# Kernel optimization log

Hardware: AMD Instinct MI355X
Metric: run time of the kernel (lower is better)

## Reference

```python
import jax, jax.numpy as jnp
import numpy as np

N = 50000      # nodes
E = 800000     # edges (avg degree 16)
IN, EMB, HID, OUT = 128, 256, 256, 128
KS = (25000, 12500)  # absolute top-k node counts per pooling level
NEG = -1e9


def setup_inputs() -> dict:
    key = jax.random.key(0)
    k = jax.random.split(key, 20)
    s = 0.05
    rn = lambda kk, shp: (jax.random.normal(kk, shp, jnp.float32) * s)
    return {
        "features": jax.random.normal(k[0], (N, IN), jnp.float32),
        "src": jax.random.randint(k[1], (E,), 0, N, dtype=jnp.int32),
        "dst": jax.random.randint(k[2], (E,), 0, N, dtype=jnp.int32),
        "W_embed": rn(k[3], (IN, EMB)), "b_embed": jnp.zeros((EMB,), jnp.float32),
        "W_enc0": rn(k[4], (EMB, HID)), "b_enc0": jnp.zeros((HID,), jnp.float32),
        "W_enc1": rn(k[5], (HID, HID)), "b_enc1": jnp.zeros((HID,), jnp.float32),
        "W_p0": rn(k[6], (HID, 1)), "b_p0": jnp.zeros((1,), jnp.float32),
        "W_p1": rn(k[7], (HID, 1)), "b_p1": jnp.zeros((1,), jnp.float32),
        "W_bot": rn(k[8], (HID, HID)), "b_bot": jnp.zeros((HID,), jnp.float32),
        "W_dec0": rn(k[9], (HID, HID)), "b_dec0": jnp.zeros((HID,), jnp.float32),
        "W_dec1": rn(k[10], (HID, OUT)), "b_dec1": jnp.zeros((OUT,), jnp.float32),
    }


def _gcn(h, src, dst, emask, W, b, act):
    """DGL GraphConv, norm='both': D_out^{-1/2} A D_in^{-1/2} h W + b, deg clamped >=1.
    emask: float [E] validity mask for edges of the current (sub)graph."""
    n = h.shape[0]
    deg_out = jnp.clip(jax.ops.segment_sum(emask, src, num_segments=n), 1.0)
    deg_in = jnp.clip(jax.ops.segment_sum(emask, dst, num_segments=n), 1.0)
    msg = (h * (deg_out ** -0.5)[:, None])[src] * emask[:, None]  # [E, F]
    agg = jax.ops.segment_sum(msg, dst, num_segments=n)
    out = (agg * (deg_in ** -0.5)[:, None]) @ W + b
    return jax.nn.relu(out) if act else out


def _forward(features, src, dst, W_embed, b_embed, W_enc0, b_enc0, W_enc1, b_enc1,
             W_p0, b_p0, W_p1, b_p1, W_bot, b_bot, W_dec0, b_dec0, W_dec1, b_dec1):
    n = features.shape[0]
    ones_e = jnp.ones((src.shape[0],), features.dtype)
    enc = [(W_enc0, b_enc0), (W_enc1, b_enc1)]
    pools = [(W_p0, b_p0), (W_p1, b_p1)]
    dec = [(W_dec0, b_dec0), (W_dec1, b_dec1)]
    L = len(KS)

    h = _gcn(features, src, dst, ones_e, W_embed, b_embed, True)
    masks = [jnp.ones((n,), features.dtype)]  # node mask per graph level
    hidden = []
    for i in range(L):  # encoder (dropout = eval-mode identity)
        m = masks[i]
        em = m[src] * m[dst]
        h = _gcn(h, src, dst, em, enc[i][0], enc[i][1], True) * m[:, None]
        hidden.append(h)
        # gPool: sigmoid projection score, top-k node selection, gate by score
        scores = jax.nn.sigmoid(h @ pools[i][0] + pools[i][1])[:, 0]
        _, idx = jax.lax.top_k(jnp.where(m > 0, scores, NEG), KS[i])
        nm = jnp.zeros((n,), features.dtype).at[idx].set(1.0)
        h = h * (scores * nm)[:, None]
        masks.append(nm)
    mL = masks[L]
    emL = mL[src] * mL[dst]
    h = _gcn(h, src, dst, emL, W_bot, b_bot, True) * mL[:, None]
    for i in range(L):  # decoder: gUnpool (identity under full-rep masking) + skip + GCN
        j = L - 1 - i
        h = h + hidden[j]
        m = masks[j]
        em = m[src] * m[dst]
        act = i < L - 1  # last decoder layer has no activation
        h = _gcn(h, src, dst, em, dec[i][0], dec[i][1], act) * m[:, None]
    return h


def reference(features, src, dst, W_embed, b_embed, W_enc0, b_enc0, W_enc1, b_enc1,
              W_p0, b_p0, W_p1, b_p1, W_bot, b_bot, W_dec0, b_dec0, W_dec1, b_dec1):
    return _forward(features, src, dst, W_embed, b_embed, W_enc0, b_enc0, W_enc1, b_enc1,
                    W_p0, b_p0, W_p1, b_p1, W_bot, b_bot, W_dec0, b_dec0, W_dec1, b_dec1)
```

## Files before the change

kernel.cpp:

```cpp
#include <hip/hip_runtime.h>
#include <hip/hip_bf16.h>
#include <type_traits>

__global__ void hist_kernel(const int* __restrict__ src, const int* __restrict__ dst,
                            int* __restrict__ deg_out, int* __restrict__ deg_in, int E) {
    int e = blockIdx.x * blockDim.x + threadIdx.x;
    if (e < E) {
        atomicAdd(&deg_out[src[e]], 1);
        atomicAdd(&deg_in[dst[e]], 1);
    }
}

__global__ void scan_kernel(const int* __restrict__ deg, int* __restrict__ row_ptr,
                            int* __restrict__ cursor, int n) {
    __shared__ int wsum[16];
    __shared__ int running;
    int tid = threadIdx.x, lane = tid & 63, wid = tid >> 6;
    if (tid == 0) running = 0;
    __syncthreads();
    for (int base = 0; base < n; base += 1024) {
        int i = base + tid;
        int v = (i < n) ? deg[i] : 0;
        int incl = v;
        #pragma unroll
        for (int off = 1; off < 64; off <<= 1) {
            int t = __shfl_up(incl, off);
            if (lane >= off) incl += t;
        }
        if (lane == 63) wsum[wid] = incl;
        __syncthreads();
        if (wid == 0 && lane < 16) {
            int s = wsum[lane], si = s;
            #pragma unroll
            for (int off = 1; off < 16; off <<= 1) {
                int t = __shfl_up(si, off);
                if (lane >= off) si += t;
            }
            wsum[lane] = si - s;
        }
        __syncthreads();
        int excl = running + wsum[wid] + (incl - v);
        if (i < n) { row_ptr[i] = excl; cursor[i] = excl; }
        __syncthreads();
        if (tid == 1023) running = excl + v;
        __syncthreads();
    }
    if (tid == 0) row_ptr[n] = running;
}

__global__ void fill_kernel(const int* __restrict__ src, const int* __restrict__ dst,
                            int* __restrict__ cursor, int* __restrict__ col, int E) {
    int e = blockIdx.x * blockDim.x + threadIdx.x;
    if (e < E) {
        int p = atomicAdd(&cursor[dst[e]], 1);
        col[p] = src[e];
    }
}

__global__ void sort_rows_kernel(const int* __restrict__ row_ptr, int* __restrict__ col, int n) {
    int v = blockIdx.x * blockDim.x + threadIdx.x;
    if (v >= n) return;
    int e0 = row_ptr[v], e1 = row_ptr[v + 1];
    for (int i = e0 + 1; i < e1; ++i) {
        int key = col[i];
        int j = i - 1;
        while (j >= e0 && col[j] > key) { col[j + 1] = col[j]; --j; }
        col[j + 1] = key;
    }
}

__global__ void out_deg_mask_kernel(const int* __restrict__ src, const int* __restrict__ dst,
                                    const float* __restrict__ m, float* __restrict__ so, int E) {
    int e = blockIdx.x * blockDim.x + threadIdx.x;
    if (e < E) {
        float md = m[dst[e]];
        if (md != 0.f) atomicAdd(&so[src[e]], md);
    }
}

__global__ void in_deg_mask_kernel(const int* __restrict__ row_ptr, const int* __restrict__ col,
                                   const float* __restrict__ m, float* __restrict__ si, int n) {
    int v = blockIdx.x * blockDim.x + threadIdx.x;
    if (v < n) {
        float s = 0.f;
        int e1 = row_ptr[v + 1];
        for (int e = row_ptr[v]; e < e1; ++e) s += m[col[e]];
        si[v] = s;
    }
}

__global__ void scale_full_kernel(const int* __restrict__ dout, const int* __restrict__ din,
                                  float* __restrict__ s, float* __restrict__ t, int n) {
    int v = blockIdx.x * blockDim.x + threadIdx.x;
    if (v < n) {
        s[v] = 1.f / sqrtf((float)max(dout[v], 1));
        t[v] = 1.f / sqrtf((float)max(din[v], 1));
    }
}

__global__ void scale_mask_kernel(const float* __restrict__ gate, const float* __restrict__ mask,
                                  const float* __restrict__ so, const float* __restrict__ si,
                                  float* __restrict__ s, float* __restrict__ t, int n) {
    int v = blockIdx.x * blockDim.x + threadIdx.x;
    if (v < n) {
        s[v] = gate[v] * (1.f / sqrtf(fmaxf(so[v], 1.f)));
        t[v] = mask[v] * (1.f / sqrtf(fmaxf(si[v], 1.f)));
    }
}

__global__ void agg_feat_128_kernel(const int* __restrict__ row_ptr, const int* __restrict__ col,
                                    const float* __restrict__ X, const float* __restrict__ s,
                                    const float* __restrict__ t, float* __restrict__ out, int n) {
    int tid = threadIdx.x;
    int node = blockIdx.x * 8 + (tid >> 5);
    int f4 = tid & 31;
    if (node >= n) return;
    int e0 = row_ptr[node], e1 = row_ptr[node + 1];
    const float4* X4 = (const float4*)X;
    float ax = 0.f, ay = 0.f, az = 0.f, aw = 0.f;
    int e = e0;
    for (; e + 3 < e1; e += 4) {
        int u0 = col[e], u1 = col[e + 1], u2 = col[e + 2], u3 = col[e + 3];
        float s0 = s[u0], s1 = s[u1], s2 = s[u2], s3 = s[u3];
        float4 x0 = X4[(size_t)u0 * 32 + f4];
        float4 x1 = X4[(size_t)u1 * 32 + f4];
        float4 x2 = X4[(size_t)u2 * 32 + f4];
        float4 x3 = X4[(size_t)u3 * 32 + f4];
        ax += s0 * x0.x; ay += s0 * x0.y; az += s0 * x0.z; aw += s0 * x0.w;
        ax += s1 * x1.x; ay += s1 * x1.y; az += s1 * x1.z; aw += s1 * x1.w;
        ax += s2 * x2.x; ay += s2 * x2.y; az += s2 * x2.z; aw += s2 * x2.w;
        ax += s3 * x3.x; ay += s3 * x3.y; az += s3 * x3.z; aw += s3 * x3.w;
    }
    for (; e < e1; ++e) {
        int u = col[e];
        float sc = s[u];
        float4 q = X4[(size_t)u * 32 + f4];
        ax += sc * q.x; ay += sc * q.y; az += sc * q.z; aw += sc * q.w;
    }
    float tv = t[node];
    float4 r; r.x = ax * tv; r.y = ay * tv; r.z = az * tv; r.w = aw * tv;
    ((float4*)out)[(size_t)node * 32 + f4] = r;
}

template <bool MASKED>
__global__ void agg_f32_256_kernel(const int* __restrict__ row_ptr, const int* __restrict__ col,
                                   const float* __restrict__ X, const float* __restrict__ s,
                                   const float* __restrict__ t, float* __restrict__ out, int n) {
    int tid = threadIdx.x;
    int node = blockIdx.x * 4 + (tid >> 6);
    int f4 = tid & 63;
    if (node >= n) return;
    float tv = t[node];
    if (MASKED && tv == 0.f) return;
    int e0 = row_ptr[node], e1 = row_ptr[node + 1];
    const float4* X4 = (const float4*)X;
    float ax = 0.f, ay = 0.f, az = 0.f, aw = 0.f;
    int e = e0;
    for (; e + 3 < e1; e += 4) {
        int u0 = col[e], u1 = col[e + 1], u2 = col[e + 2], u3 = col[e + 3];
        float s0 = s[u0], s1 = s[u1], s2 = s[u2], s3 = s[u3];
        if (!MASKED) {
            float4 x0 = X4[(size_t)u0 * 64 + f4];
            float4 x1 = X4[(size_t)u1 * 64 + f4];
            float4 x2 = X4[(size_t)u2 * 64 + f4];
            float4 x3 = X4[(size_t)u3 * 64 + f4];
            ax += s0 * x0.x; ay += s0 * x0.y; az += s0 * x0.z; aw += s0 * x0.w;
            ax += s1 * x1.x; ay += s1 * x1.y; az += s1 * x1.z; aw += s1 * x1.w;
            ax += s2 * x2.x; ay += s2 * x2.y; az += s2 * x2.z; aw += s2 * x2.w;
            ax += s3 * x3.x; ay += s3 * x3.y; az += s3 * x3.z; aw += s3 * x3.w;
        } else {
            if (s0 != 0.f) { float4 x = X4[(size_t)u0 * 64 + f4];
                ax += s0 * x.x; ay += s0 * x.y; az += s0 * x.z; aw += s0 * x.w; }
            if (s1 != 0.f) { float4 x = X4[(size_t)u1 * 64 + f4];
                ax += s1 * x.x; ay += s1 * x.y; az += s1 * x.z; aw += s1 * x.w; }
            if (s2 != 0.f) { float4 x = X4[(size_t)u2 * 64 + f4];
                ax += s2 * x.x; ay += s2 * x.y; az += s2 * x.z; aw += s2 * x.w; }
            if (s3 != 0.f) { float4 x = X4[(size_t)u3 * 64 + f4];
                ax += s3 * x.x; ay += s3 * x.y; az += s3 * x.z; aw += s3 * x.w; }
        }
    }
    for (; e < e1; ++e) {
        int u = col[e];
        float sc = s[u];
        if (!MASKED || sc != 0.f) {
            float4 xv = X4[(size_t)u * 64 + f4];
            ax += sc * xv.x; ay += sc * xv.y; az += sc * xv.z; aw += sc * xv.w;
        }
    }
    float4 r; r.x = ax * tv; r.y = ay * tv; r.z = az * tv; r.w = aw * tv;
    ((float4*)out)[(size_t)node * 64 + f4] = r;
}

__global__ void agg_bias_128_kernel(const int* __restrict__ row_ptr, const int* __restrict__ col,
                                    const float* __restrict__ P, const float* __restrict__ t,
                                    const float* __restrict__ bias, float* __restrict__ out, int n) {
    int tid = threadIdx.x;
    int node = blockIdx.x * 8 + (tid >> 5);
    int f4 = tid & 31;
    if (node >= n) return;
    int e0 = row_ptr[node], e1 = row_ptr[node + 1];
    const float4* P4 = (const float4*)P;
    float ax = 0.f, ay = 0.f, az = 0.f, aw = 0.f;
    int e = e0;
    for (; e + 3 < e1; e += 4) {
        int u0 = col[e], u1 = col[e + 1], u2 = col[e + 2], u3 = col[e + 3];
        float4 x0 = P4[(size_t)u0 * 32 + f4];
        float4 x1 = P4[(size_t)u1 * 32 + f4];
        float4 x2 = P4[(size_t)u2 * 32 + f4];
        float4 x3 = P4[(size_t)u3 * 32 + f4];
        ax += x0.x; ay += x0.y; az += x0.z; aw += x0.w;
        ax += x1.x; ay += x1.y; az += x1.z; aw += x1.w;
        ax += x2.x; ay += x2.y; az += x2.z; aw += x2.w;
        ax += x3.x; ay += x3.y; az += x3.z; aw += x3.w;
    }
    for (; e < e1; ++e) {
        int u = col[e];
        float4 q = P4[(size_t)u * 32 + f4];
        ax += q.x; ay += q.y; az += q.z; aw += q.w;
    }
    float tv = t[node];
    float4 bv = ((const float4*)bias)[f4];
    float4 r;
    r.x = ax * tv + bv.x; r.y = ay * tv + bv.y;
    r.z = az * tv + bv.z; r.w = aw * tv + bv.w;
    ((float4*)out)[(size_t)node * 32 + f4] = r;
}

template <bool RELU>
__global__ __launch_bounds__(256) void gemm_kernel(const float* __restrict__ A,
                                                   const float* __restrict__ W,
                                                   const float* __restrict__ bias,
                                                   const float* __restrict__ mask,
                                                   const float* __restrict__ rowscale,
                                                   float* __restrict__ C, int M, int K, int Nn) {
    __shared__ float As[16][68];
    __shared__ float Bs[16][132];
    int tid = threadIdx.x;
    int bm = blockIdx.x * 64, bn = blockIdx.y * 128;
    int mA = tid >> 2, kqA = (tid & 3) * 4;
    int kB = tid >> 4, nqB = (tid & 15) * 8;
    int tm = (tid >> 4) * 4, tn = (tid & 15) * 4;
    float acc[4][8] = {};
    float rs = rowscale ? rowscale[bm + mA] : 1.f;
    for (int k0 = 0; k0 < K; k0 += 16) {
        float4 av = *(const float4*)(A + (size_t)(bm + mA) * K + k0 + kqA);
        As[kqA + 0][mA] = av.x * rs; As[kqA + 1][mA] = av.y * rs;
        As[kqA + 2][mA] = av.z * rs; As[kqA + 3][mA] = av.w * rs;
        const float* wp = W + (size_t)(k0 + kB) * Nn + bn + nqB;
        *(float4*)&Bs[kB][nqB]     = *(const float4*)wp;
        *(float4*)&Bs[kB][nqB + 4] = *(const float4*)(wp + 4);
        __syncthreads();
        #pragma unroll
        for (int kk = 0; kk < 16; ++kk) {
            float4 a  = *(const float4*)&As[kk][tm];
            float4 b0 = *(const float4*)&Bs[kk][tn];
            float4 b1 = *(const float4*)&Bs[kk][tn + 64];
            float ar[4] = {a.x, a.y, a.z, a.w};
            float br[8] = {b0.x, b0.y, b0.z, b0.w, b1.x, b1.y, b1.z, b1.w};
            #pragma unroll
            for (int i2 = 0; i2 < 4; i2++)
                #pragma unroll
                for (int j = 0; j < 8; j++) acc[i2][j] += ar[i2] * br[j];
        }
        __syncthreads();
    }
    #pragma unroll
    for (int i2 = 0; i2 < 4; i2++) {
        int row = bm + tm + i2;
        if (row < M) {
            float mv = mask ? mask[row] : 1.f;
            float o[8];
            #pragma unroll
            for (int j = 0; j < 8; j++) {
                int cj = (j < 4) ? (tn + j) : (64 + tn + j - 4);
                float x = acc[i2][j] + (bias ? bias[bn + cj] : 0.f);
                if (RELU) x = fmaxf(x, 0.f);
                o[j] = x * mv;
            }
            float* cp = C + (size_t)row * Nn + bn;
            *(float4*)(cp + tn)      = make_float4(o[0], o[1], o[2], o[3]);
            *(float4*)(cp + 64 + tn) = make_float4(o[4], o[5], o[6], o[7]);
        }
    }
}

template <bool RELU>
__global__ __launch_bounds__(256) void gemm_rows_kernel(const float* __restrict__ A,
                                                        const float* __restrict__ W,
                                                        const float* __restrict__ bias,
                                                        const int* __restrict__ idx, int Mc,
                                                        float* __restrict__ C, int K, int Nn) {
    __shared__ float As[16][68];
    __shared__ float Bs[16][132];
    __shared__ int ridx[64];
    int tid = threadIdx.x;
    int bm = blockIdx.x * 64, bn = blockIdx.y * 128;
    if (tid < 64) {
        int r = bm + tid;
        ridx[tid] = (r < Mc) ? idx[r] : idx[0];
    }
    __syncthreads();
    int mA = tid >> 2, kqA = (tid & 3) * 4;
    int kB = tid >> 4, nqB = (tid & 15) * 8;
    int tm = (tid >> 4) * 4, tn = (tid & 15) * 4;
    int rA = ridx[mA];
    float acc[4][8] = {};
    for (int k0 = 0; k0 < K; k0 += 16) {
        float4 av = *(const float4*)(A + (size_t)rA * K + k0 + kqA);
        As[kqA + 0][mA] = av.x; As[kqA + 1][mA] = av.y;
        As[kqA + 2][mA] = av.z; As[kqA + 3][mA] = av.w;
        const float* wp = W + (size_t)(k0 + kB) * Nn + bn + nqB;
        *(float4*)&Bs[kB][nqB]     = *(const float4*)wp;
        *(float4*)&Bs[kB][nqB + 4] = *(const float4*)(wp + 4);
        __syncthreads();
        #pragma unroll
        for (int kk = 0; kk < 16; ++kk) {
            float4 a  = *(const float4*)&As[kk][tm];
            float4 b0 = *(const float4*)&Bs[kk][tn];
            float4 b1 = *(const float4*)&Bs[kk][tn + 64];
            float ar[4] = {a.x, a.y, a.z, a.w};
            float br[8] = {b0.x, b0.y, b0.z, b0.w, b1.x, b1.y, b1.z, b1.w};
            #pragma unroll
            for (int i2 = 0; i2 < 4; i2++)
                #pragma unroll
                for (int j = 0; j < 8; j++) acc[i2][j] += ar[i2] * br[j];
        }
        __syncthreads();
    }
    #pragma unroll
    for (int i2 = 0; i2 < 4; i2++) {
        int r = bm + tm + i2;
        if (r < Mc) {
            int row = ridx[tm + i2];
            float o[8];
            #pragma unroll
            for (int j = 0; j < 8; j++) {
                int cj = (j < 4) ? (tn + j) : (64 + tn + j - 4);
                float x = acc[i2][j] + bias[bn + cj];
                if (RELU) x = fmaxf(x, 0.f);
                o[j] = x;
            }
            float* cp = C + (size_t)row * Nn + bn;
            *(float4*)(cp + tn)      = make_float4(o[0], o[1], o[2], o[3]);
            *(float4*)(cp + 64 + tn) = make_float4(o[4], o[5], o[6], o[7]);
        }
    }
}

__global__ void score_kernel(const float* __restrict__ H, const float* __restrict__ Wp,
                             const float* __restrict__ bp, const float* __restrict__ mask,
                             float* __restrict__ scores, float* __restrict__ keys, int n) {
    int lane = threadIdx.x & 63;
    int node = blockIdx.x * 4 + (threadIdx.x >> 6);
    if (node >= n) return;
    float4 hv = ((const float4*)(H + (size_t)node * 256))[lane];
    float4 wq = ((const float4*)Wp)[lane];
    float d = hv.x * wq.x + hv.y * wq.y + hv.z * wq.z + hv.w * wq.w;
    #pragma unroll
    for (int off = 32; off > 0; off >>= 1) d += __shfl_down(d, off);
    if (lane == 0) {
        float sc = 1.f / (1.f + expf(-(d + bp[0])));
        scores[node] = sc;
        keys[node] = (mask && mask[node] == 0.f) ? -1e9f : sc;
    }
}

__device__ __forceinline__ unsigned key_u(float f) {
    unsigned u = __float_as_uint(f);
    return (u & 0x80000000u) ? ~u : (u | 0x80000000u);
}

__device__ __forceinline__ void wave_hist_add(int* __restrict__ hist, unsigned bin, bool valid) {
    int lane = threadIdx.x & 63;
    while (true) {
        unsigned long long vmask = __ballot(valid);
        if (vmask == 0ull) break;
        int leader = __ffsll((long long)vmask) - 1;
        unsigned lbin = (unsigned)__shfl((int)bin, leader);
        bool match = valid && (bin == lbin);
        unsigned long long mmask = __ballot(match);
        if (lane == leader) atomicAdd(&hist[lbin], __popcll(mmask));
        if (match) valid = false;
    }
}

__global__ void topk_kernel(const float* __restrict__ keys, const float* __restrict__ scores,
                            float* __restrict__ nm, float* __restrict__ gate, int n, int K) {
    __shared__ int hist[256];
    __shared__ unsigned sh_prefix;
    __shared__ int sh_krem;
    __shared__ int sh_running;
    __shared__ int wsum[16];
    int tid = threadIdx.x, lane = tid & 63, wid = tid >> 6;
    if (tid == 0) { sh_prefix = 0u; sh_krem = K; sh_running = 0; }
    __syncthreads();
    for (int pass = 0; pass < 4; ++pass) {
        int shift = 24 - pass * 8;
        if (tid < 256) hist[tid] = 0;
        __syncthreads();
        unsigned pmask = (pass == 0) ? 0u : (0xFFFFFFFFu << (shift + 8));
        unsigned prefix = sh_prefix;
        for (int i = tid; i < n; i += 1024) {
            unsigned u = key_u(keys[i]);
            if ((u & pmask) == prefix) atomicAdd(&hist[(u >> shift) & 0xFF], 1);
        }
        __syncthreads();
        if (tid == 0) {
            int krem = sh_krem;
            int b;
            for (b = 255; b > 0; --b) {
                int c = hist[b];
                if (c >= krem) break;
                krem -= c;
            }
            sh_prefix = prefix | ((unsigned)b << shift);
            sh_krem = krem;
        }
        __syncthreads();
    }
    unsigned Tkey = sh_prefix;
    int need_eq = sh_krem;
    for (int base = 0; base < n; base += 1024) {
        int i = base + tid;
        unsigned u = 0; int flagv = 0;
        if (i < n) { u = key_u(keys[i]); flagv = (u == Tkey) ? 1 : 0; }
        unsigned long long bal = __ballot(flagv);
        int rank_w = __popcll(bal & ((1ull << lane) - 1ull));
        if (lane == 63) wsum[wid] = __popcll(bal);
        __syncthreads();
        int woff = 0;
        for (int w = 0; w < wid; ++w) woff += wsum[w];
        int grank = sh_running + woff + rank_w;
        if (i < n) {
            float v = (u > Tkey) ? 1.f : ((flagv && grank < need_eq) ? 1.f : 0.f);
            nm[i] = v;
            gate[i] = v * scores[i];
        }
        __syncthreads();
        if (tid == 0) {
            int tot = 0;
            for (int w = 0; w < 16; ++w) tot += wsum[w];
            sh_running += tot;
        }
        __syncthreads();
    }
}

__global__ void topk_hist1(const float* __restrict__ keys, int n, int* __restrict__ hist) {
    int i = blockIdx.x * blockDim.x + threadIdx.x;
    unsigned bin = 0; bool valid = (i < n);
    if (valid) bin = key_u(keys[i]) >> 16;
    wave_hist_add(hist, bin, valid);
}

__global__ void topk_scan1(const int* __restrict__ hist, int K, int* __restrict__ sel) {
    __shared__ int arr[1024];
    int tid = threadIdx.x;
    int base = tid * 64;
    int local = 0;
    #pragma unroll 8
    for (int b = 0; b < 64; ++b) local += hist[base + b];
    arr[tid] = local;
    __syncthreads();
    for (int off = 1; off < 1024; off <<= 1) {
        int v = (tid + off < 1024) ? arr[tid + off] : 0;
        __syncthreads();
        arr[tid] += v;
        __syncthreads();
    }
    int above = arr[tid] - local;
    if (above < K && arr[tid] >= K) {
        int run = above;
        for (int b = base + 63; b >= base; --b) {
            int c = hist[b];
            if (run + c >= K) { sel[0] = b; sel[1] = K - run; break; }
            run += c;
        }
    }
}

__global__ void topk_hist2(const float* __restrict__ keys, int n, const int* __restrict__ sel,
                           int* __restrict__ hist) {
    int i = blockIdx.x * blockDim.x + threadIdx.x;
    unsigned bin = 0; bool valid = false;
    if (i < n) {
        unsigned u = key_u(keys[i]);
        if ((int)(u >> 16) == sel[0]) { bin = u & 0xFFFF; valid = true; }
    }
    wave_hist_add(hist, bin, valid);
}

__global__ void topk_scan2(const int* __restrict__ hist, int* __restrict__ sel,
                           int* __restrict__ tie_cnt) {
    __shared__ int arr[1024];
    int tid = threadIdx.x;
    if (tid == 0) *tie_cnt = 0;
    int K = sel[1];
    int base = tid * 64;
    int local = 0;
    #pragma unroll 8
    for (int b = 0; b < 64; ++b) local += hist[base + b];
    arr[tid] = local;
    __syncthreads();
    for (int off = 1; off < 1024; off <<= 1) {
        int v = (tid + off < 1024) ? arr[tid + off] : 0;
        __syncthreads();
        arr[tid] += v;
        __syncthreads();
    }
    int above = arr[tid] - local;
    if (above < K && arr[tid] >= K) {
        int run = above;
        for (int b = base + 63; b >= base; --b) {
            int c = hist[b];
            if (run + c >= K) {
                sel[2] = (int)((((unsigned)sel[0]) << 16) | (unsigned)b);
                sel[3] = K - run;
                break;
            }
            run += c;
        }
    }
}

__global__ void topk_mark(const float* __restrict__ keys, const float* __restrict__ scores,
                          const int* __restrict__ sel, float* __restrict__ nm,
                          float* __restrict__ gate, int* __restrict__ tie_list,
                          int* __restrict__ tie_cnt, int n) {
    int i = blockIdx.x * blockDim.x + threadIdx.x;
    if (i >= n) return;
    unsigned Tkey = (unsigned)sel[2];
    unsigned u = key_u(keys[i]);
    float v = 0.f;
    if (u > Tkey) v = 1.f;
    else if (u == Tkey) { int p = atomicAdd(tie_cnt, 1); tie_list[p] = i; }
    nm[i] = v;
    gate[i] = v * scores[i];
}

__global__ void topk_ties(const float* __restrict__ scores, const int* __restrict__ sel,
                          const int* __restrict__ tie_list, const int* __restrict__ tie_cnt,
                          float* __restrict__ nm, float* __restrict__ gate) {
    int cnt = *tie_cnt;
    int need = sel[3];
    for (int j = threadIdx.x; j < cnt; j += blockDim.x) {
        int idx = tie_list[j];
        int rank = 0;
        for (int k2 = 0; k2 < cnt; ++k2) rank += (tie_list[k2] < idx) ? 1 : 0;
        if (rank < need) { nm[idx] = 1.f; gate[idx] = scores[idx]; }
    }
}

__global__ void compact_kernel(const float* __restrict__ nm, int* __restrict__ idx,
                               int* __restrict__ cnt, int n) {
    int i = blockIdx.x * blockDim.x + threadIdx.x;
    if (i < n && nm[i] != 0.f) {
        int p = atomicAdd(cnt, 1);
        idx[p] = i;
    }
}

__global__ void add_mask_kernel(float* __restrict__ A, const float* __restrict__ B,
                                const float* __restrict__ mask, int n4) {
    int i = blockIdx.x * blockDim.x + threadIdx.x;
    if (i < n4) {
        float4 a = ((float4*)A)[i];
        float4 b = ((const float4*)B)[i];
        if (mask && mask[i >> 6] == 0.f) { a.x = 0.f; a.y = 0.f; a.z = 0.f; a.w = 0.f; }
        a.x += b.x; a.y += b.y; a.z += b.z; a.w += b.w;
        ((float4*)A)[i] = a;
    }
}

extern "C" void kernel_launch(void* const* d_in, const int* in_sizes, int n_in,
                              void* d_out, int out_size, void* d_ws, size_t ws_size,
                              hipStream_t stream) {
    const int n = in_sizes[0] / 128;
    const int E = in_sizes[1];
    const int NPAD = ((n + 63) / 64) * 64;
    const int K1 = 25000, K2 = 12500;

    const float* features = (const float*)d_in[0];
    const int* src = (const int*)d_in[1];
    const int* dst = (const int*)d_in[2];
    const float* W_embed = (const float*)d_in[3];
    const float* b_embed = (const float*)d_in[4];
    const float* W_enc0  = (const float*)d_in[5];
    const float* b_enc0  = (const float*)d_in[6];
    const float* W_enc1  = (const float*)d_in[7];
    const float* b_enc1  = (const float*)d_in[8];
    const float* W_p0    = (const float*)d_in[9];
    const float* b_p0    = (const float*)d_in[10];
    const float* W_p1    = (const float*)d_in[11];
    const float* b_p1    = (const float*)d_in[12];
    const float* W_bot   = (const float*)d_in[13];
    const float* b_bot   = (const float*)d_in[14];
    const float* W_dec0  = (const float*)d_in[15];
    const float* b_dec0  = (const float*)d_in[16];
    const float* W_dec1  = (const float*)d_in[17];
    const float* b_dec1  = (const float*)d_in[18];
    float* out_f = (float*)d_out;

    char* ws = (char*)d_ws;
    size_t off = 0;
    auto alloc = [&](size_t bytes) -> void* {
        void* p = ws + off;
        off += (bytes + 255) & ~(size_t)255;
        return p;
    };
    (void)alloc(256);
    int* row_ptr  = (int*)alloc((size_t)(n + 1) * 4);
    int* cursor   = (int*)alloc((size_t)n * 4);
    int* col      = (int*)alloc((size_t)E * 4);
    int* deg_out_i= (int*)alloc((size_t)n * 4);
    int* deg_in_i = (int*)alloc((size_t)n * 4);
    float* so_m1  = (float*)alloc((size_t)n * 4);
    float* si_m1  = (float*)alloc((size_t)n * 4);
    float* so_m2  = (float*)alloc((size_t)n * 4);
    float* si_m2  = (float*)alloc((size_t)n * 4);
    float* sarr   = (float*)alloc((size_t)n * 4);
    float* tarr   = (float*)alloc((size_t)n * 4);
    float* scores1= (float*)alloc((size_t)n * 4);
    float* keys1  = (float*)alloc((size_t)n * 4);
    float* scores2= (float*)alloc((size_t)n * 4);
    float* keys2  = (float*)alloc((size_t)n * 4);
    float* nm1    = (float*)alloc((size_t)n * 4);
    float* gate1  = (float*)alloc((size_t)n * 4);
    float* nm2    = (float*)alloc((size_t)n * 4);
    float* gate2  = (float*)alloc((size_t)n * 4);
    size_t big = (size_t)NPAD * 256 * 4;
    float* A = (float*)alloc(big);
    float* B = (float*)alloc(big);
    float* C = (float*)alloc(big);
    float* D = (float*)alloc(big);
    int* rhist    = (int*)alloc(65536 * 4);
    int* sel      = (int*)alloc(256);
    int* tie_cnt  = (int*)alloc(256);
    int* tie_list = (int*)alloc((size_t)n * 4);
    float* s0     = (float*)alloc((size_t)n * 4);
    float* t0     = (float*)alloc((size_t)n * 4);
    int* idx1     = (int*)alloc((size_t)n * 4);
    int* idx2     = (int*)alloc((size_t)n * 4);
    int* ccnt     = (int*)alloc(256);
    bool fast = (off <= ws_size);

    dim3 blk(256);
    int gE = (E + 255) / 256;
    int gN = (n + 255) / 256;
    int gAgg256 = (n + 3) / 4;
    int gAgg128 = (n + 7) / 8;
    int gScore = (n + 3) / 4;
    dim3 gemm_g(NPAD / 64, 2);
    dim3 gemm_g128(NPAD / 64, 1);
    dim3 gemm_gK1((K1 + 63) / 64, 2);
    dim3 gemm_gK2((K2 + 63) / 64, 2);
    int gAdd = (n * 64 + 255) / 256;

    auto run_topk = [&](const float* keys, const float* scores, float* nm, float* gate, int K) {
        if (fast) {
            hipMemsetAsync(rhist, 0, 65536 * 4, stream);
            topk_hist1<<<gN, blk, 0, stream>>>(keys, n, rhist);
            topk_scan1<<<1, 1024, 0, stream>>>(rhist, K, sel);
            hipMemsetAsync(rhist, 0, 65536 * 4, stream);
            topk_hist2<<<gN, blk, 0, stream>>>(keys, n, sel, rhist);
            topk_scan2<<<1, 1024, 0, stream>>>(rhist, sel, tie_cnt);
            topk_mark<<<gN, blk, 0, stream>>>(keys, scores, sel, nm, gate, tie_list, tie_cnt, n);
            topk_ties<<<1, 256, 0, stream>>>(scores, sel, tie_list, tie_cnt, nm, gate);
        } else {
            topk_kernel<<<1, 1024, 0, stream>>>(keys, scores, nm, gate, n, K);
        }
    };
    float* sF = fast ? s0 : sarr;
    float* tF = fast ? t0 : tarr;

    hipMemsetAsync(deg_out_i, 0, (size_t)n * 4, stream);
    hipMemsetAsync(deg_in_i, 0, (size_t)n * 4, stream);
    hist_kernel<<<gE, blk, 0, stream>>>(src, dst, deg_out_i, deg_in_i, E);
    scan_kernel<<<1, 1024, 0, stream>>>(deg_in_i, row_ptr, cursor, n);
    fill_kernel<<<gE, blk, 0, stream>>>(src, dst, cursor, col, E);
    sort_rows_kernel<<<gN, blk, 0, stream>>>(row_ptr, col, n);

    scale_full_kernel<<<gN, blk, 0, stream>>>(deg_out_i, deg_in_i, sF, tF, n);

    agg_feat_128_kernel<<<gAgg128, blk, 0, stream>>>(row_ptr, col, features, sF, tF, D, n);
    gemm_kernel<true><<<gemm_g, blk, 0, stream>>>(D, W_embed, b_embed, nullptr, nullptr, A, n, 128, 256);

    agg_f32_256_kernel<false><<<gAgg256, blk, 0, stream>>>(row_ptr, col, A, sF, tF, D, n);
    gemm_kernel<true><<<gemm_g, blk, 0, stream>>>(D, W_enc0, b_enc0, nullptr, nullptr, B, n, 256, 256);

    score_kernel<<<gScore, blk, 0, stream>>>(B, W_p0, b_p0, nullptr, scores1, keys1, n);
    run_topk(keys1, scores1, nm1, gate1, K1);
    if (fast) {
        hipMemsetAsync(ccnt, 0, 4, stream);
        compact_kernel<<<gN, blk, 0, stream>>>(nm1, idx1, ccnt, n);
    }

    hipMemsetAsync(so_m1, 0, (size_t)n * 4, stream);
    out_deg_mask_kernel<<<gE, blk, 0, stream>>>(src, dst, nm1, so_m1, E);
    in_deg_mask_kernel<<<gN, blk, 0, stream>>>(row_ptr, col, nm1, si_m1, n);
    scale_mask_kernel<<<gN, blk, 0, stream>>>(gate1, nm1, so_m1, si_m1, sarr, tarr, n);
    agg_f32_256_kernel<true><<<gAgg256, blk, 0, stream>>>(row_ptr, col, B, sarr, tarr, D, n);
    if (fast)
        gemm_rows_kernel<true><<<gemm_gK1, blk, 0, stream>>>(D, W_enc1, b_enc1, idx1, K1, C, 256, 256);
    else
        gemm_kernel<true><<<gemm_g, blk, 0, stream>>>(D, W_enc1, b_enc1, nm1, nullptr, C, n, 256, 256);

    score_kernel<<<gScore, blk, 0, stream>>>(C, W_p1, b_p1, nm1, scores2, keys2, n);
    run_topk(keys2, scores2, nm2, gate2, K2);
    if (fast) {
        hipMemsetAsync(ccnt + 1, 0, 4, stream);
        compact_kernel<<<gN, blk, 0, stream>>>(nm2, idx2, ccnt + 1, n);
    }

    hipMemsetAsync(so_m2, 0, (size_t)n * 4, stream);
    out_deg_mask_kernel<<<gE, blk, 0, stream>>>(src, dst, nm2, so_m2, E);
    in_deg_mask_kernel<<<gN, blk, 0, stream>>>(row_ptr, col, nm2, si_m2, n);
    scale_mask_kernel<<<gN, blk, 0, stream>>>(gate2, nm2, so_m2, si_m2, sarr, tarr, n);
    agg_f32_256_kernel<true><<<gAgg256, blk, 0, stream>>>(row_ptr, col, C, sarr, tarr, D, n);
    if (fast)
        gemm_rows_kernel<true><<<gemm_gK2, blk, 0, stream>>>(D, W_bot, b_bot, idx2, K2, A, 256, 256);
    else
        gemm_kernel<true><<<gemm_g, blk, 0, stream>>>(D, W_bot, b_bot, nm2, nullptr, A, n, 256, 256);

    add_mask_kernel<<<gAdd, blk, 0, stream>>>(A, C, fast ? nm2 : nullptr, n * 64);
    scale_mask_kernel<<<gN, blk, 0, stream>>>(nm1, nm1, so_m1, si_m1, sarr, tarr, n);
    agg_f32_256_kernel<true><<<gAgg256, blk, 0, stream>>>(row_ptr, col, A, sarr, tarr, D, n);
    if (fast)
        gemm_rows_kernel<true><<<gemm_gK1, blk, 0, stream>>>(D, W_dec0, b_dec0, idx1, K1, A, 256, 256);
    else
        gemm_kernel<true><<<gemm_g, blk, 0, stream>>>(D, W_dec0, b_dec0, nm1, nullptr, A, n, 256, 256);

    add_mask_kernel<<<gAdd, blk, 0, stream>>>(A, B, fast ? nm1 : nullptr, n * 64);
    if (!fast)
        scale_full_kernel<<<gN, blk, 0, stream>>>(deg_out_i, deg_in_i, sarr, tarr, n);
    gemm_kernel<false><<<gemm_g128, blk, 0, stream>>>(A, W_dec1, nullptr, nullptr, sF, C, n, 256, 128);
    agg_bias_128_kernel<<<gAgg128, blk, 0, stream>>>(row_ptr, col, C, tF, b_dec1, out_f, n);

    (void)n_in; (void)out_size;
}
```

Measured before the change: 1.312 ms.

## Aggregate only selected rows, build CSR by source, fuse compaction into top-k

Adds a source-sorted CSR so masked out-degrees can be computed by gather inside one fused deg_scale kernel, replacing the atomic edge pass, a memset and separate in-degree and scale kernels. Aggregation now runs only over the compacted top-k node indices instead of all n nodes. Compaction is folded into topk_mark and topk_ties, and the histogram is cleared inside the scan kernels instead of by memsets. The cost is an extra scan and fill to build the second CSR, plus nondeterministic order of the compacted index list.

```diff
diff --git a/kernel.cpp b/kernel.cpp
--- a/kernel.cpp
+++ b/kernel.cpp
@@ -48,12 +48,12 @@
     if (tid == 0) row_ptr[n] = running;
 }
 
-__global__ void fill_kernel(const int* __restrict__ src, const int* __restrict__ dst,
+__global__ void fill_kernel(const int* __restrict__ a, const int* __restrict__ b,
                             int* __restrict__ cursor, int* __restrict__ col, int E) {
     int e = blockIdx.x * blockDim.x + threadIdx.x;
     if (e < E) {
-        int p = atomicAdd(&cursor[dst[e]], 1);
-        col[p] = src[e];
+        int p = atomicAdd(&cursor[b[e]], 1);
+        col[p] = a[e];
     }
 }
 
@@ -106,6 +106,25 @@
         s[v] = gate[v] * (1.f / sqrtf(fmaxf(so[v], 1.f)));
         t[v] = mask[v] * (1.f / sqrtf(fmaxf(si[v], 1.f)));
     }
+}
+
+__global__ void deg_scale_kernel(const int* __restrict__ rp_s, const int* __restrict__ cs,
+                                 const int* __restrict__ rp_d, const int* __restrict__ cd,
+                                 const float* __restrict__ gate, const float* __restrict__ mask,
+                                 float* __restrict__ s, float* __restrict__ t,
+                                 float* __restrict__ so_out, float* __restrict__ si_out, int n) {
+    int v = blockIdx.x * blockDim.x + threadIdx.x;
+    if (v >= n) return;
+    float so = 0.f;
+    int e1 = rp_s[v + 1];
+    for (int e = rp_s[v]; e < e1; ++e) so += mask[cs[e]];
+    float si = 0.f;
+    e1 = rp_d[v + 1];
+    for (int e = rp_d[v]; e < e1; ++e) si += mask[cd[e]];
+    s[v] = gate[v] * (1.f / sqrtf(fmaxf(so, 1.f)));
+    t[v] = mask[v] * (1.f / sqrtf(fmaxf(si, 1.f)));
+    so_out[v] = so;
+    si_out[v] = si;
 }
 
 __global__ void agg_feat_128_kernel(const int* __restrict__ row_ptr, const int* __restrict__ col,
@@ -191,6 +210,44 @@
     ((float4*)out)[(size_t)node * 64 + f4] = r;
 }
 
+__global__ void agg_rows_256_kernel(const int* __restrict__ row_ptr, const int* __restrict__ col,
+                                    const float* __restrict__ X, const float* __restrict__ s,
+                                    const float* __restrict__ t, const int* __restrict__ idx,
+                                    int Mc, float* __restrict__ out) {
+    int tid = threadIdx.x;
+    int li = blockIdx.x * 4 + (tid >> 6);
+    int f4 = tid & 63;
+    if (li >= Mc) return;
+    int node = idx[li];
+    float tv = t[node];
+    int e0 = row_ptr[node], e1 = row_ptr[node + 1];
+    const float4* X4 = (const float4*)X;
+    float ax = 0.f, ay = 0.f, az = 0.f, aw = 0.f;
+    int e = e0;
+    for (; e + 3 < e1; e += 4) {
+        int u0 = col[e], u1 = col[e + 1], u2 = col[e + 2], u3 = col[e + 3];
+        float s0 = s[u0], s1 = s[u1], s2 = s[u2], s3 = s[u3];
+        if (s0 != 0.f) { float4 x = X4[(size_t)u0 * 64 + f4];
+            ax += s0 * x.x; ay += s0 * x.y; az += s0 * x.z; aw += s0 * x.w; }
+        if (s1 != 0.f) { float4 x = X4[(size_t)u1 * 64 + f4];
+            ax += s1 * x.x; ay += s1 * x.y; az += s1 * x.z; aw += s1 * x.w; }
+        if (s2 != 0.f) { float4 x = X4[(size_t)u2 * 64 + f4];
+            ax += s2 * x.x; ay += s2 * x.y; az += s2 * x.z; aw += s2 * x.w; }
+        if (s3 != 0.f) { float4 x = X4[(size_t)u3 * 64 + f4];
+            ax += s3 * x.x; ay += s3 * x.y; az += s3 * x.z; aw += s3 * x.w; }
+    }
+    for (; e < e1; ++e) {
+        int u = col[e];
+        float sc = s[u];
+        if (sc != 0.f) {
+            float4 xv = X4[(size_t)u * 64 + f4];
+            ax += sc * xv.x; ay += sc * xv.y; az += sc * xv.z; aw += sc * xv.w;
+        }
+    }
+    float4 r; r.x = ax * tv; r.y = ay * tv; r.z = az * tv; r.w = aw * tv;
+    ((float4*)out)[(size_t)node * 64 + f4] = r;
+}
+
 __global__ void agg_bias_128_kernel(const int* __restrict__ row_ptr, const int* __restrict__ col,
                                     const float* __restrict__ P, const float* __restrict__ t,
                                     const float* __restrict__ bias, float* __restrict__ out, int n) {
@@ -453,7 +510,7 @@
     wave_hist_add(hist, bin, valid);
 }
 
-__global__ void topk_scan1(const int* __restrict__ hist, int K, int* __restrict__ sel) {
+__global__ void topk_scan1(int* __restrict__ hist, int K, int* __restrict__ sel) {
     __shared__ int arr[1024];
     int tid = threadIdx.x;
     int base = tid * 64;
@@ -477,6 +534,8 @@
             run += c;
         }
     }
+    #pragma unroll 8
+    for (int b = 0; b < 64; ++b) hist[base + b] = 0;
 }
 
 __global__ void topk_hist2(const float* __restrict__ keys, int n, const int* __restrict__ sel,
@@ -490,11 +549,11 @@
     wave_hist_add(hist, bin, valid);
 }
 
-__global__ void topk_scan2(const int* __restrict__ hist, int* __restrict__ sel,
-                           int* __restrict__ tie_cnt) {
+__global__ void topk_scan2(int* __restrict__ hist, int* __restrict__ sel,
+                           int* __restrict__ tie_cnt, int* __restrict__ ccnt) {
     __shared__ int arr[1024];
     int tid = threadIdx.x;
-    if (tid == 0) *tie_cnt = 0;
+    if (tid == 0) { *tie_cnt = 0; *ccnt = 0; }
     int K = sel[1];
     int base = tid * 64;
     int local = 0;
@@ -521,18 +580,21 @@
             run += c;
         }
     }
+    #pragma unroll 8
+    for (int b = 0; b < 64; ++b) hist[base + b] = 0;
 }
 
 __global__ void topk_mark(const float* __restrict__ keys, const float* __restrict__ scores,
                           const int* __restrict__ sel, float* __restrict__ nm,
                           float* __restrict__ gate, int* __restrict__ tie_list,
-                          int* __restrict__ tie_cnt, int n) {
+                          int* __restrict__ tie_cnt, int* __restrict__ sidx,
+                          int* __restrict__ ccnt, int n) {
     int i = blockIdx.x * blockDim.x + threadIdx.x;
     if (i >= n) return;
     unsigned Tkey = (unsigned)sel[2];
     unsigned u = key_u(keys[i]);
     float v = 0.f;
-    if (u > Tkey) v = 1.f;
+    if (u > Tkey) { v = 1.f; int p = atomicAdd(ccnt, 1); sidx[p] = i; }
     else if (u == Tkey) { int p = atomicAdd(tie_cnt, 1); tie_list[p] = i; }
     nm[i] = v;
     gate[i] = v * scores[i];
@@ -540,23 +602,18 @@
 
 __global__ void topk_ties(const float* __restrict__ scores, const int* __restrict__ sel,
                           const int* __restrict__ tie_list, const int* __restrict__ tie_cnt,
-                          float* __restrict__ nm, float* __restrict__ gate) {
+                          float* __restrict__ nm, float* __restrict__ gate,
+                          int* __restrict__ sidx, int* __restrict__ ccnt) {
     int cnt = *tie_cnt;
     int need = sel[3];
     for (int j = threadIdx.x; j < cnt; j += blockDim.x) {
         int idx = tie_list[j];
         int rank = 0;
         for (int k2 = 0; k2 < cnt; ++k2) rank += (tie_list[k2] < idx) ? 1 : 0;
-        if (rank < need) { nm[idx] = 1.f; gate[idx] = scores[idx]; }
-    }
-}
-
-__global__ void compact_kernel(const float* __restrict__ nm, int* __restrict__ idx,
-                               int* __restrict__ cnt, int n) {
-    int i = blockIdx.x * blockDim.x + threadIdx.x;
-    if (i < n && nm[i] != 0.f) {
-        int p = atomicAdd(cnt, 1);
-        idx[p] = i;
+        if (rank < need) {
+            nm[idx] = 1.f; gate[idx] = scores[idx];
+            int p = atomicAdd(ccnt, 1); sidx[p] = idx;
+        }
     }
 }
 
@@ -642,6 +699,9 @@
     int* idx1     = (int*)alloc((size_t)n * 4);
     int* idx2     = (int*)alloc((size_t)n * 4);
     int* ccnt     = (int*)alloc(256);
+    int* row_ptr_s= (int*)alloc((size_t)(n + 1) * 4);
+    int* cursor_s = (int*)alloc((size_t)n * 4);
+    int* col_s    = (int*)alloc((size_t)E * 4);
     bool fast = (off <= ws_size);
 
     dim3 blk(256);
@@ -649,6 +709,8 @@
     int gN = (n + 255) / 256;
     int gAgg256 = (n + 3) / 4;
     int gAgg128 = (n + 7) / 8;
+    int gAggK1 = (K1 + 3) / 4;
+    int gAggK2 = (K2 + 3) / 4;
     int gScore = (n + 3) / 4;
     dim3 gemm_g(NPAD / 64, 2);
     dim3 gemm_g128(NPAD / 64, 1);
@@ -656,16 +718,16 @@
     dim3 gemm_gK2((K2 + 63) / 64, 2);
     int gAdd = (n * 64 + 255) / 256;
 
-    auto run_topk = [&](const float* keys, const float* scores, float* nm, float* gate, int K) {
+    auto run_topk = [&](const float* keys, const float* scores, float* nm, float* gate,
+                        int K, int* sidx, int* cc) {
         if (fast) {
-            hipMemsetAsync(rhist, 0, 65536 * 4, stream);
             topk_hist1<<<gN, blk, 0, stream>>>(keys, n, rhist);
             topk_scan1<<<1, 1024, 0, stream>>>(rhist, K, sel);
-            hipMemsetAsync(rhist, 0, 65536 * 4, stream);
             topk_hist2<<<gN, blk, 0, stream>>>(keys, n, sel, rhist);
-            topk_scan2<<<1, 1024, 0, stream>>>(rhist, sel, tie_cnt);
-            topk_mark<<<gN, blk, 0, stream>>>(keys, scores, sel, nm, gate, tie_list, tie_cnt, n);
-            topk_ties<<<1, 256, 0, stream>>>(scores, sel, tie_list, tie_cnt, nm, gate);
+            topk_scan2<<<1, 1024, 0, stream>>>(rhist, sel, tie_cnt, cc);
+            topk_mark<<<gN, blk, 0, stream>>>(keys, scores, sel, nm, gate, tie_list, tie_cnt,
+                                              sidx, cc, n);
+            topk_ties<<<1, 256, 0, stream>>>(scores, sel, tie_list, tie_cnt, nm, gate, sidx, cc);
         } else {
             topk_kernel<<<1, 1024, 0, stream>>>(keys, scores, nm, gate, n, K);
         }
@@ -675,10 +737,15 @@
 
     hipMemsetAsync(deg_out_i, 0, (size_t)n * 4, stream);
     hipMemsetAsync(deg_in_i, 0, (size_t)n * 4, stream);
+    if (fast) hipMemsetAsync(rhist, 0, 65536 * 4, stream);
     hist_kernel<<<gE, blk, 0, stream>>>(src, dst, deg_out_i, deg_in_i, E);
     scan_kernel<<<1, 1024, 0, stream>>>(deg_in_i, row_ptr, cursor, n);
     fill_kernel<<<gE, blk, 0, stream>>>(src, dst, cursor, col, E);
     sort_rows_kernel<<<gN, blk, 0, stream>>>(row_ptr, col, n);
+    if (fast) {
+        scan_kernel<<<1, 1024, 0, stream>>>(deg_out_i, row_ptr_s, cursor_s, n);
+        fill_kernel<<<gE, blk, 0, stream>>>(dst, src, cursor_s, col_s, E);
+    }
 
     scale_full_kernel<<<gN, blk, 0, stream>>>(deg_out_i, deg_in_i, sF, tF, n);
 
@@ -689,46 +756,48 @@
     gemm_kernel<true><<<gemm_g, blk, 0, stream>>>(D, W_enc0, b_enc0, nullptr, nullptr, B, n, 256, 256);
 
     score_kernel<<<gScore, blk, 0, stream>>>(B, W_p0, b_p0, nullptr, scores1, keys1, n);
-    run_topk(keys1, scores1, nm1, gate1, K1);
+    run_topk(keys1, scores1, nm1, gate1, K1, idx1, ccnt);
+
     if (fast) {
-        hipMemsetAsync(ccnt, 0, 4, stream);
-        compact_kernel<<<gN, blk, 0, stream>>>(nm1, idx1, ccnt, n);
-    }
-
-    hipMemsetAsync(so_m1, 0, (size_t)n * 4, stream);
-    out_deg_mask_kernel<<<gE, blk, 0, stream>>>(src, dst, nm1, so_m1, E);
-    in_deg_mask_kernel<<<gN, blk, 0, stream>>>(row_ptr, col, nm1, si_m1, n);
-    scale_mask_kernel<<<gN, blk, 0, stream>>>(gate1, nm1, so_m1, si_m1, sarr, tarr, n);
-    agg_f32_256_kernel<true><<<gAgg256, blk, 0, stream>>>(row_ptr, col, B, sarr, tarr, D, n);
-    if (fast)
+        deg_scale_kernel<<<gN, blk, 0, stream>>>(row_ptr_s, col_s, row_ptr, col, gate1, nm1,
+                                                 sarr, tarr, so_m1, si_m1, n);
+        agg_rows_256_kernel<<<gAggK1, blk, 0, stream>>>(row_ptr, col, B, sarr, tarr, idx1, K1, D);
         gemm_rows_kernel<true><<<gemm_gK1, blk, 0, stream>>>(D, W_enc1, b_enc1, idx1, K1, C, 256, 256);
-    else
+    } else {
+        hipMemsetAsync(so_m1, 0, (size_t)n * 4, stream);
+        out_deg_mask_kernel<<<gE, blk, 0, stream>>>(src, dst, nm1, so_m1, E);
+        in_deg_mask_kernel<<<gN, blk, 0, stream>>>(row_ptr, col, nm1, si_m1, n);
+        scale_mask_kernel<<<gN, blk, 0, stream>>>(gate1, nm1, so_m1, si_m1, sarr, tarr, n);
+        agg_f32_256_kernel<true><<<gAgg256, blk, 0, stream>>>(row_ptr, col, B, sarr, tarr, D, n);
         gemm_kernel<true><<<gemm_g, blk, 0, stream>>>(D, W_enc1, b_enc1, nm1, nullptr, C, n, 256, 256);
+    }
 
     score_kernel<<<gScore, blk, 0, stream>>>(C, W_p1, b_p1, nm1, scores2, keys2, n);
-    run_topk(keys2, scores2, nm2, gate2, K2);
+    run_topk(keys2, scores2, nm2, gate2, K2, idx2, ccnt + 1);
+
     if (fast) {
-        hipMemsetAsync(ccnt + 1, 0, 4, stream);
-        compact_kernel<<<gN, blk, 0, stream>>>(nm2, idx2, ccnt + 1, n);
-    }
-
-    hipMemsetAsync(so_m2, 0, (size_t)n * 4, stream);
-    out_deg_mask_kernel<<<gE, blk, 0, stream>>>(src, dst, nm2, so_m2, E);
-    in_deg_mask_kernel<<<gN, blk, 0, stream>>>(row_ptr, col, nm2, si_m2, n);
-    scale_mask_kernel<<<gN, blk, 0, stream>>>(gate2, nm2, so_m2, si_m2, sarr, tarr, n);
-    agg_f32_256_kernel<true><<<gAgg256, blk, 0, stream>>>(row_ptr, col, C, sarr, tarr, D, n);
-    if (fast)
+        deg_scale_kernel<<<gN, blk, 0, stream>>>(row_ptr_s, col_s, row_ptr, col, gate2, nm2,
+                                                 sarr, tarr, so_m2, si_m2, n);
+        agg_rows_256_kernel<<<gAggK2, blk, 0, stream>>>(row_ptr, col, C, sarr, tarr, idx2, K2, D);
         gemm_rows_kernel<true><<<gemm_gK2, blk, 0, stream>>>(D, W_bot, b_bot, idx2, K2, A, 256, 256);
-    else
+    } else {
+        hipMemsetAsync(so_m2, 0, (size_t)n * 4, stream);
+        out_deg_mask_kernel<<<gE, blk, 0, stream>>>(src, dst, nm2, so_m2, E);
+        in_deg_mask_kernel<<<gN, blk, 0, stream>>>(row_ptr, col, nm2, si_m2, n);
+        scale_mask_kernel<<<gN, blk, 0, stream>>>(gate2, nm2, so_m2, si_m2, sarr, tarr, n);
+        agg_f32_256_kernel<true><<<gAgg256, blk, 0, stream>>>(row_ptr, col, C, sarr, tarr, D, n);
         gemm_kernel<true><<<gemm_g, blk, 0, stream>>>(D, W_bot, b_bot, nm2, nullptr, A, n, 256, 256);
+    }
 
     add_mask_kernel<<<gAdd, blk, 0, stream>>>(A, C, fast ? nm2 : nullptr, n * 64);
     scale_mask_kernel<<<gN, blk, 0, stream>>>(nm1, nm1, so_m1, si_m1, sarr, tarr, n);
-    agg_f32_256_kernel<true><<<gAgg256, blk, 0, stream>>>(row_ptr, col, A, sarr, tarr, D, n);
-    if (fast)
+    if (fast) {
+        agg_rows_256_kernel<<<gAggK1, blk, 0, stream>>>(row_ptr, col, A, sarr, tarr, idx1, K1, D);
         gemm_rows_kernel<true><<<gemm_gK1, blk, 0, stream>>>(D, W_dec0, b_dec0, idx1, K1, A, 256, 256);
-    else
+    } else {
+        agg_f32_256_kernel<true><<<gAgg256, blk, 0, stream>>>(row_ptr, col, A, sarr, tarr, D, n);
         gemm_kernel<true><<<gemm_g, blk, 0, stream>>>(D, W_dec0, b_dec0, nm1, nullptr, A, n, 256, 256);
+    }
 
     add_mask_kernel<<<gAdd, blk, 0, stream>>>(A, B, fast ? nm1 : nullptr, n * 64);
     if (!fast)
```

After: 1.792 ms. +36.6%, slower.
